# Kernel tuning notes

Hardware: AMD Instinct MI355X
Metric: run time of the kernel (lower is better)

The kernel has to match this reference:

```python
import jax, jax.numpy as jnp
import numpy as np

N = 30000       # nodes
E = 480000      # edges (before self-loops)
G = 64          # graphs in batch
IN = 128        # in_channels
HID = 128       # hidden_dim
HEADS = 4
NEG_SLOPE = 0.2


def gat_layer(x, src, dst, W, att_src, att_dst, b):
    """PyG-style GATConv: W [Fin, H*C], att_* [H, C], b [H*C]. Returns [N, H*C] (head concat)."""
    H, C = att_src.shape
    h = (x @ W).reshape(-1, H, C)                      # [N, H, C]
    a_s = jnp.einsum('nhc,hc->nh', h, att_src)         # [N, H]
    a_d = jnp.einsum('nhc,hc->nh', h, att_dst)
    e = jax.nn.leaky_relu(a_s[src] + a_d[dst], NEG_SLOPE)   # [Etot, H]
    # segment softmax over edges grouped by destination node
    m = jax.ops.segment_max(e, dst, num_segments=N)
    e = jnp.exp(e - m[dst])
    denom = jax.ops.segment_sum(e, dst, num_segments=N)
    alpha = e / (denom[dst] + 1e-16)                   # [Etot, H]
    msg = h[src] * alpha[:, :, None]                   # [Etot, H, C]
    out = jax.ops.segment_sum(msg, dst, num_segments=N)
    return out.reshape(-1, H * C) + b


def setup_inputs():
    key = jax.random.key(0)
    ks = jax.random.split(key, 13)
    s = 0.05
    x = jax.random.normal(ks[0], (N, IN), jnp.float32)
    edge_index = jax.random.randint(ks[1], (2, E), 0, N, dtype=jnp.int32)
    batch = jnp.sort(jax.random.randint(ks[2], (N,), 0, G, dtype=jnp.int32))
    return {
        'x': x,
        'edge_index': edge_index,
        'batch': batch,
        'W1': jax.random.normal(ks[3], (IN, HEADS * HID), jnp.float32) * s,
        'att_src1': jax.random.normal(ks[4], (HEADS, HID), jnp.float32) * s,
        'att_dst1': jax.random.normal(ks[5], (HEADS, HID), jnp.float32) * s,
        'b1': jnp.zeros((HEADS * HID,), jnp.float32),
        'W2': jax.random.normal(ks[6], (HEADS * HID, HID), jnp.float32) * s,
        'att_src2': jax.random.normal(ks[7], (1, HID), jnp.float32) * s,
        'att_dst2': jax.random.normal(ks[8], (1, HID), jnp.float32) * s,
        'b2': jnp.zeros((HID,), jnp.float32),
        'lin_w': jax.random.normal(ks[9], (HID, 1), jnp.float32) * s,
        'lin_b': jnp.zeros((1,), jnp.float32),
    }


def reference(x, edge_index, batch, W1, att_src1, att_dst1, b1, W2, att_src2, att_dst2, b2, lin_w, lin_b):
    # add self-loops (PyG GATConv default)
    loop = jnp.arange(N, dtype=edge_index.dtype)
    src = jnp.concatenate([edge_index[0], loop])
    dst = jnp.concatenate([edge_index[1], loop])

    h = gat_layer(x, src, dst, W1, att_src1, att_dst1, b1)   # [N, 4*HID]
    h = jax.nn.elu(h)
    h = gat_layer(h, src, dst, W2, att_src2, att_dst2, b2)   # [N, HID]
    h = jax.nn.elu(h)

    # global mean pool over graphs
    sums = jax.ops.segment_sum(h, batch, num_segments=G)     # [G, HID]
    cnts = jax.ops.segment_sum(jnp.ones((N,), h.dtype), batch, num_segments=G)
    pooled = sums / jnp.maximum(cnts, 1.0)[:, None]

    out = pooled @ lin_w + lin_b                             # [G, 1]
    return out.squeeze(-1)                                   # [G]
```

## Files before the change

### kernel.cpp

```cpp
#include <hip/hip_runtime.h>

#define NN    30000
#define EE    480000
#define ETOT  (EE + NN)
#define GG    64
#define IN_CH 128
#define HID   128
#define HEADS 4
#define F1    (HEADS * HID)
#define CAP   64

typedef __attribute__((ext_vector_type(8))) __bf16 bf16x8;
typedef __attribute__((ext_vector_type(4))) float  floatx4;
typedef __attribute__((ext_vector_type(2))) float  f32x2;

__device__ __forceinline__ float lrelu(float x) { return x > 0.f ? x : 0.2f * x; }
__device__ __forceinline__ float elu_f(float x) { return x > 0.f ? x : (expf(x) - 1.f); }
__device__ __forceinline__ unsigned short f2bf(float f) {
    unsigned int u = __float_as_uint(f);
    return (unsigned short)((u + 0x7FFFu + ((u >> 16) & 1u)) >> 16);
}
__device__ __forceinline__ float bf2f(unsigned short u) {
    return __uint_as_float(((unsigned int)u) << 16);
}
__device__ __forceinline__ f32x2 fma2(float a, f32x2 v, f32x2 acc) {
    f32x2 av = {a, a};
    return __builtin_elementwise_fma(av, v, acc);
}

__device__ __forceinline__ float wred_sum(float v) {
#pragma unroll
    for (int off = 32; off; off >>= 1) v += __shfl_xor(v, off);
    return v;
}

#define LDKC 136
__global__ __launch_bounds__(256) void gemm_bf16(const unsigned short* __restrict__ A, int lda, int zA,
                                                 const unsigned short* __restrict__ Bt, int zBt, int K,
                                                 unsigned short* __restrict__ C, int ldc, int zC,
                                                 const float* __restrict__ bias, int zBias,
                                                 int M, int do_elu)
{
    A  += (size_t)blockIdx.z * zA;
    Bt += (size_t)blockIdx.z * zBt;
    C  += (size_t)blockIdx.z * zC;
    const float* bias_p = bias ? bias + (size_t)blockIdx.z * zBias : nullptr;

    __shared__ unsigned short Bl[128 * LDKC];

    const int tid  = threadIdx.x;
    const int wave = tid >> 6, lane = tid & 63;
    const int quad = lane >> 4, l16 = lane & 15;
    const int bm = blockIdx.x * 128;

    floatx4 zf = {0.f, 0.f, 0.f, 0.f};
    floatx4 acc[2][8];
#pragma unroll
    for (int rt = 0; rt < 2; rt++)
#pragma unroll
        for (int ct = 0; ct < 8; ct++) acc[rt][ct] = zf;

    float bb[8];
#pragma unroll
    for (int ct = 0; ct < 8; ct++) bb[ct] = bias_p ? bias_p[ct * 16 + l16] : 0.f;

    const int r0 = bm + wave * 32 + l16;
    const int r1 = r0 + 16;

    for (int kc = 0; kc < K; kc += 128) {
        uint4 av[2][4];
#pragma unroll
        for (int kb = 0; kb < 4; kb++) {
            const int k = kc + kb * 32 + quad * 8;
            av[0][kb] = (r0 < M) ? *(const uint4*)(A + (size_t)r0 * lda + k) : uint4{0,0,0,0};
            av[1][kb] = (r1 < M) ? *(const uint4*)(A + (size_t)r1 * lda + k) : uint4{0,0,0,0};
        }

        if (kc) __syncthreads();
#pragma unroll
        for (int i = 0; i < 8; i++) {
            int j = i * 256 + tid;
            int n = j >> 4, ko = (j & 15) * 8;
            *(uint4*)&Bl[n * LDKC + ko] = *(const uint4*)(Bt + (size_t)n * K + kc + ko);
        }
        __syncthreads();

#pragma unroll
        for (int kb = 0; kb < 4; kb++) {
            bf16x8 bfr[8];
#pragma unroll
            for (int ct = 0; ct < 8; ct++)
                bfr[ct] = *(bf16x8*)&Bl[(ct * 16 + l16) * LDKC + kb * 32 + quad * 8];
            bf16x8 a0 = *(bf16x8*)&av[0][kb];
            bf16x8 a1 = *(bf16x8*)&av[1][kb];
#pragma unroll
            for (int ct = 0; ct < 8; ct++) {
                acc[0][ct] = __builtin_amdgcn_mfma_f32_16x16x32_bf16(a0, bfr[ct], acc[0][ct], 0, 0, 0);
                acc[1][ct] = __builtin_amdgcn_mfma_f32_16x16x32_bf16(a1, bfr[ct], acc[1][ct], 0, 0, 0);
            }
        }
    }

    __syncthreads();
    unsigned short* wls = Bl + wave * (16 * 128);
#pragma unroll
    for (int rt = 0; rt < 2; rt++) {
        if (rt) __builtin_amdgcn_wave_barrier();
#pragma unroll
        for (int ct = 0; ct < 8; ct++) {
#pragma unroll
            for (int reg = 0; reg < 4; reg++) {
                float v = acc[rt][ct][reg] + bb[ct];
                if (do_elu) v = elu_f(v);
                wls[(quad * 4 + reg) * 128 + ct * 16 + l16] = f2bf(v);
            }
        }
        __builtin_amdgcn_wave_barrier();
#pragma unroll
        for (int i = 0; i < 4; i++) {
            int j = i * 64 + lane;
            int rl = j >> 4, off = (j & 15) * 8;
            int row = bm + wave * 32 + rt * 16 + rl;
            if (row < M)
                *(uint4*)(C + (size_t)row * ldc + off) = *(uint4*)&wls[rl * 128 + off];
        }
    }
}

__global__ void cast_bf16_k(const float* __restrict__ src, unsigned short* __restrict__ dst, int npairs)
{
    int i = blockIdx.x * 256 + threadIdx.x;
    if (i < npairs) {
        float2 v = *(const float2*)(src + (size_t)i * 2);
        *(unsigned int*)(dst + (size_t)i * 2) =
            (unsigned)f2bf(v.x) | ((unsigned)f2bf(v.y) << 16);
    }
}

__global__ void prep_k(const float* __restrict__ W1, const float* __restrict__ W2,
                       const float* __restrict__ att_s, const float* __restrict__ att_d,
                       unsigned short* __restrict__ W1t, unsigned short* __restrict__ W2t,
                       float* __restrict__ wt)
{
    int b = blockIdx.x;
    if (b < 256) {
        int idx = b * 256 + threadIdx.x;
        int h = idx >> 14, rem = idx & 16383, n = rem >> 7, k = rem & 127;
        W1t[idx] = f2bf(W1[(size_t)k * F1 + h * 128 + n]);
    } else if (b < 512) {
        int idx = (b - 256) * 256 + threadIdx.x;
        int n = idx >> 9, k = idx & 511;
        W2t[idx] = f2bf(W2[(size_t)k * HID + n]);
    } else if (threadIdx.x < 128) {
        int q = b - 512;
        int h = q & 3, sd = q >> 2;
        int i = threadIdx.x;
        const float* att = (sd ? att_d : att_s) + h * 128;
        const float* wr = W1 + (size_t)i * F1 + h * 128;
        float acc = 0.f;
        for (int c = 0; c < 128; c++) acc = fmaf(wr[c], att[c], acc);
        wt[sd * 512 + h * 128 + i] = acc;
    }
}

__global__ __launch_bounds__(128) void score1_k(const float* __restrict__ x,
                                                const float* __restrict__ wt,
                                                float* __restrict__ a_s,
                                                float* __restrict__ a_d)
{
    __shared__ __align__(16) float swt[1024];
    int t = threadIdx.x;
    ((float4*)swt)[t]       = ((const float4*)wt)[t];
    ((float4*)swt)[t + 128] = ((const float4*)wt)[t + 128];
    __syncthreads();
    int node = blockIdx.x * 16 + (t >> 3);
    int q = t & 7;
    int h = q & 3, sd = q >> 2;
    if (node >= NN) return;
    const float4* xr = (const float4*)(x + (size_t)node * IN_CH);
    const float4* wr = (const float4*)(swt + sd * 512 + h * 128);
    float acc = 0.f;
#pragma unroll 4
    for (int c = 0; c < 32; c++) {
        float4 xv = xr[c], wv = wr[c];
        acc = fmaf(xv.x, wv.x, acc);
        acc = fmaf(xv.y, wv.y, acc);
        acc = fmaf(xv.z, wv.z, acc);
        acc = fmaf(xv.w, wv.w, acc);
    }
    if (sd == 0) a_s[node * 4 + h] = acc;
    else         a_d[node * 4 + h] = acc;
}

__global__ __launch_bounds__(256) void att_scores_k(const unsigned short* __restrict__ h16,
                                                    const float* __restrict__ w_s,
                                                    const float* __restrict__ w_d,
                                                    float* __restrict__ a_s,
                                                    float* __restrict__ a_d)
{
    int n = blockIdx.x * 4 + (threadIdx.x >> 6);
    if (n >= NN) return;
    int l = threadIdx.x & 63;
    const unsigned short* hr = h16 + (size_t)n * 128;
    float h0 = bf2f(hr[l]), h1 = bf2f(hr[l + 64]);
    float vs = wred_sum(h0 * w_s[l] + h1 * w_s[l + 64]);
    float vd = wred_sum(h0 * w_d[l] + h1 * w_d[l + 64]);
    if (l == 0) { a_s[n] = vs; a_d[n] = vd; }
}

__global__ void fill_k(const int* __restrict__ ei, int* __restrict__ deg, int* __restrict__ perm)
{
    int i = blockIdx.x * blockDim.x + threadIdx.x;
    if (i < ETOT) {
        int s, d;
        if (i < EE) { s = ei[i]; d = ei[EE + i]; }
        else        { s = i - EE; d = i - EE; }
        int p = atomicAdd(&deg[d], 1);
        if (p < CAP) perm[(size_t)d * CAP + p] = s;
    }
}

__global__ __launch_bounds__(256) void gat_agg1w(const unsigned short* __restrict__ x16,
                                                 const float* __restrict__ a_s,
                                                 const float* __restrict__ a_d,
                                                 const int* __restrict__ deg,
                                                 const int* __restrict__ perm,
                                                 unsigned short* __restrict__ agg)
{
    __shared__ int    sSrc[4][64];
    __shared__ __align__(16) float4 sE[4][64];
    const int wave = threadIdx.x >> 6;
    const int lane = threadIdx.x & 63;
    int n = blockIdx.x * 4 + wave;
    if (n >= NN) return;
    const int rem = min(deg[n], CAP);
    const float4 ad4 = *(const float4*)(a_d + (size_t)n * 4);

    f32x2 acc0 = {0.f, 0.f}, acc1 = {0.f, 0.f}, acc2 = {0.f, 0.f}, acc3 = {0.f, 0.f};
    float d0 = 0.f, d1 = 0.f, d2 = 0.f, d3 = 0.f;

    if (lane < rem) {
        int sj = perm[(size_t)n * CAP + lane];
        float4 av = *(const float4*)(a_s + (size_t)sj * 4);
        float e0 = __expf(lrelu(av.x + ad4.x));
        float e1 = __expf(lrelu(av.y + ad4.y));
        float e2 = __expf(lrelu(av.z + ad4.z));
        float e3 = __expf(lrelu(av.w + ad4.w));
        d0 = e0; d1 = e1; d2 = e2; d3 = e3;
        sSrc[wave][lane] = sj;
        sE[wave][lane] = make_float4(e0, e1, e2, e3);
    }
    __builtin_amdgcn_wave_barrier();
    for (int j = 0; j < rem; j++) {
        int s = sSrc[wave][j];
        float4 ev = sE[wave][j];
        unsigned int uv = *(const unsigned int*)(x16 + (size_t)s * IN_CH + lane * 2);
        f32x2 xv = { __uint_as_float(uv << 16), __uint_as_float(uv & 0xFFFF0000u) };
        acc0 = fma2(ev.x, xv, acc0);
        acc1 = fma2(ev.y, xv, acc1);
        acc2 = fma2(ev.z, xv, acc2);
        acc3 = fma2(ev.w, xv, acc3);
    }
    d0 = wred_sum(d0); d1 = wred_sum(d1); d2 = wred_sum(d2); d3 = wred_sum(d3);
    const float i0 = 1.f / (d0 + 1e-16f), i1 = 1.f / (d1 + 1e-16f);
    const float i2 = 1.f / (d2 + 1e-16f), i3 = 1.f / (d3 + 1e-16f);

    unsigned short* ag = agg + (size_t)n * F1 + lane * 2;
    *(unsigned int*)(ag + 0 * 128) = (unsigned)f2bf(acc0.x * i0) | ((unsigned)f2bf(acc0.y * i0) << 16);
    *(unsigned int*)(ag + 1 * 128) = (unsigned)f2bf(acc1.x * i1) | ((unsigned)f2bf(acc1.y * i1) << 16);
    *(unsigned int*)(ag + 2 * 128) = (unsigned)f2bf(acc2.x * i2) | ((unsigned)f2bf(acc2.y * i2) << 16);
    *(unsigned int*)(ag + 3 * 128) = (unsigned)f2bf(acc3.x * i3) | ((unsigned)f2bf(acc3.y * i3) << 16);
}

__global__ __launch_bounds__(256) void gat_agg2w(const unsigned short* __restrict__ h16,
                                                 const float* __restrict__ a_s,
                                                 const float* __restrict__ a_d,
                                                 const int* __restrict__ deg,
                                                 const int* __restrict__ perm,
                                                 const float* __restrict__ bias,
                                                 unsigned short* __restrict__ out16)
{
    int n = blockIdx.x * 4 + (threadIdx.x >> 6);
    if (n >= NN) return;
    const int lane = threadIdx.x & 63;
    const int rem = min(deg[n], CAP);
    const float ad = a_d[n];

    f32x2 acc = {0.f, 0.f};
    float den = 0.f;
    int sj = 0;
    float e = 0.f;
    if (lane < rem) {
        sj = perm[(size_t)n * CAP + lane];
        e = __expf(lrelu(a_s[sj] + ad));
        den = e;
    }
    for (int j = 0; j < rem; j++) {
        int   s = __shfl(sj, j);
        float a = __shfl(e, j);
        unsigned int uv = *(const unsigned int*)(h16 + (size_t)s * HID + lane * 2);
        f32x2 hv = { __uint_as_float(uv << 16), __uint_as_float(uv & 0xFFFF0000u) };
        acc = fma2(a, hv, acc);
    }
    den = wred_sum(den);
    const float inv = 1.f / (den + 1e-16f);
    float2 bb = *(const float2*)(bias + lane * 2);
    float v0 = elu_f(acc.x * inv + bb.x);
    float v1 = elu_f(acc.y * inv + bb.y);
    *(unsigned int*)(out16 + (size_t)n * HID + lane * 2) =
        (unsigned)f2bf(v0) | ((unsigned)f2bf(v1) << 16);
}

#define NPB 64
__global__ __launch_bounds__(128) void pool_seg_k(const unsigned short* __restrict__ out16,
                                                  const int* __restrict__ batch,
                                                  float* __restrict__ pooled,
                                                  float* __restrict__ cnt)
{
    int n0 = blockIdx.x * NPB;
    int n1 = min(n0 + NPB, NN);
    if (n0 >= n1) return;
    int t = threadIdx.x;
    int cur = batch[n0];
    float acc = 0.f;
    int count = 0;
    for (int n = n0; n < n1; n++) {
        int g = batch[n];
        if (g != cur) {
            atomicAdd(&pooled[cur * HID + t], acc);
            if (t == 0) atomicAdd(&cnt[cur], (float)count);
            acc = 0.f; count = 0; cur = g;
        }
        acc += bf2f(out16[(size_t)n * HID + t]);
        count++;
    }
    atomicAdd(&pooled[cur * HID + t], acc);
    if (t == 0) atomicAdd(&cnt[cur], (float)count);
}

__global__ void final_k(const float* __restrict__ pooled, const float* __restrict__ cnt,
                        const float* __restrict__ lw, const float* __restrict__ lb,
                        float* __restrict__ outp)
{
    int g = threadIdx.x;
    if (g < GG) {
        float acc = 0.f;
        for (int c = 0; c < HID; c++) acc += pooled[g * HID + c] * lw[c];
        float cc = fmaxf(cnt[g], 1.0f);
        outp[g] = acc / cc + lb[0];
    }
}

extern "C" void kernel_launch(void* const* d_in, const int* in_sizes, int n_in,
                              void* d_out, int out_size, void* d_ws, size_t ws_size,
                              hipStream_t stream)
{
    const float* x    = (const float*)d_in[0];
    const int*   ei   = (const int*)d_in[1];
    const int*   batch= (const int*)d_in[2];
    const float* W1   = (const float*)d_in[3];
    const float* as1w = (const float*)d_in[4];
    const float* ad1w = (const float*)d_in[5];
    const float* b1   = (const float*)d_in[6];
    const float* W2   = (const float*)d_in[7];
    const float* as2w = (const float*)d_in[8];
    const float* ad2w = (const float*)d_in[9];
    const float* b2   = (const float*)d_in[10];
    const float* lw   = (const float*)d_in[11];
    const float* lb   = (const float*)d_in[12];
    float* outp = (float*)d_out;

    char* w = (char*)d_ws;
    size_t off = 0;
    auto alloc = [&](size_t bytes) -> char* {
        char* p = w + off;
        off += (bytes + 255) & ~(size_t)255;
        return p;
    };
    char*  reg0   = alloc((size_t)NN * F1 * 4);
    char*  reg1   = alloc((size_t)NN * F1 * 2);
    unsigned short* x16 = (unsigned short*)alloc((size_t)NN * IN_CH * 2);
    unsigned short* W1t = (unsigned short*)alloc(65536 * 2);
    unsigned short* W2t = (unsigned short*)alloc(65536 * 2);
    float* wt1    = (float*)alloc(1024 * 4);
    float* a_s1   = (float*)alloc((size_t)NN * 4 * 4);
    float* a_d1   = (float*)alloc((size_t)NN * 4 * 4);
    float* a_s2   = (float*)alloc((size_t)NN * 4);
    float* a_d2   = (float*)alloc((size_t)NN * 4);
    int*   deg    = (int*)alloc((size_t)NN * 4);
    int*   perm   = (int*)alloc((size_t)NN * CAP * 4);
    float* pooled = (float*)alloc((size_t)GG * HID * 4);
    float* cnt    = (float*)alloc((size_t)GG * 4);

    unsigned short* agg16   = (unsigned short*)reg0;
    unsigned short* out116  = (unsigned short*)reg1;
    unsigned short* hh2_16  = (unsigned short*)reg0;
    unsigned short* out2_16 = (unsigned short*)reg0 + (size_t)NN * HID;

    hipMemsetAsync(deg, 0, (size_t)NN * 4, stream);
    hipMemsetAsync(pooled, 0, (size_t)GG * HID * 4 + 256, stream);

    cast_bf16_k<<<(NN * IN_CH / 2 + 255) / 256, 256, 0, stream>>>(x, x16, NN * IN_CH / 2);
    prep_k<<<520, 256, 0, stream>>>(W1, W2, as1w, ad1w, W1t, W2t, wt1);
    score1_k<<<(NN + 15) / 16, 128, 0, stream>>>(x, wt1, a_s1, a_d1);

    fill_k<<<(ETOT + 255) / 256, 256, 0, stream>>>(ei, deg, perm);

    gat_agg1w<<<(NN + 3) / 4, 256, 0, stream>>>(x16, a_s1, a_d1, deg, perm, agg16);
    const int MT = (NN + 127) / 128;
    gemm_bf16<<<dim3(MT, 1, 4), 256, 0, stream>>>(agg16, F1, 128, W1t, 128 * 128, 128,
                                                  out116, F1, 128, b1, 128, NN, 1);

    gemm_bf16<<<dim3(MT, 1, 1), 256, 0, stream>>>(out116, F1, 0, W2t, 0, F1,
                                                  hh2_16, HID, 0, nullptr, 0, NN, 0);
    att_scores_k<<<(NN + 3) / 4, 256, 0, stream>>>(hh2_16, as2w, ad2w, a_s2, a_d2);
    gat_agg2w<<<(NN + 3) / 4, 256, 0, stream>>>(hh2_16, a_s2, a_d2, deg, perm, b2, out2_16);

    pool_seg_k<<<(NN + NPB - 1) / NPB, 128, 0, stream>>>(out2_16, batch, pooled, cnt);
    final_k<<<1, 64, 0, stream>>>(pooled, cnt, lw, lb, outp);
}
```

Baseline: 263.7 us.

## Fuse memsets, bf16 cast, and layer-2 attention scores into neighboring kernels

Zeroing of deg and pooled/cnt moves into extra blocks of prep_k, the x→bf16 cast folds into score1_k, and the layer-2 attention-score dot products are computed in the second GEMM's epilogue from its LDS tile. The softmax denominators are now built from the broadcast per-edge values inside the aggregation loops, which removes the wave reductions. The aim is fewer kernel launches and fewer passes over global memory. In exchange, the GEMM epilogue does more work and the cast in score1_k uses scalar bf16 stores.

```diff
diff --git a/kernel.cpp b/kernel.cpp
--- a/kernel.cpp
+++ b/kernel.cpp
@@ -28,18 +28,16 @@
     return __builtin_elementwise_fma(av, v, acc);
 }
 
-__device__ __forceinline__ float wred_sum(float v) {
-#pragma unroll
-    for (int off = 32; off; off >>= 1) v += __shfl_xor(v, off);
-    return v;
-}
-
 #define LDKC 136
 __global__ __launch_bounds__(256) void gemm_bf16(const unsigned short* __restrict__ A, int lda, int zA,
                                                  const unsigned short* __restrict__ Bt, int zBt, int K,
                                                  unsigned short* __restrict__ C, int ldc, int zC,
                                                  const float* __restrict__ bias, int zBias,
-                                                 int M, int do_elu)
+                                                 int M, int do_elu,
+                                                 const float* __restrict__ ws,
+                                                 const float* __restrict__ wd,
+                                                 float* __restrict__ as_out,
+                                                 float* __restrict__ ad_out)
 {
     A  += (size_t)blockIdx.z * zA;
     Bt += (size_t)blockIdx.z * zBt;
@@ -124,23 +122,28 @@
             if (row < M)
                 *(uint4*)(C + (size_t)row * ldc + off) = *(uint4*)&wls[rl * 128 + off];
         }
-    }
-}
-
-__global__ void cast_bf16_k(const float* __restrict__ src, unsigned short* __restrict__ dst, int npairs)
-{
-    int i = blockIdx.x * 256 + threadIdx.x;
-    if (i < npairs) {
-        float2 v = *(const float2*)(src + (size_t)i * 2);
-        *(unsigned int*)(dst + (size_t)i * 2) =
-            (unsigned)f2bf(v.x) | ((unsigned)f2bf(v.y) << 16);
+        if (ws) {
+            int row = bm + wave * 32 + rt * 16 + l16;
+            const unsigned short* rowp = &wls[l16 * 128 + quad * 32];
+            float ps = 0.f, pd = 0.f;
+#pragma unroll
+            for (int jj = 0; jj < 32; jj++) {
+                float hv = bf2f(rowp[jj]);
+                ps = fmaf(hv, ws[quad * 32 + jj], ps);
+                pd = fmaf(hv, wd[quad * 32 + jj], pd);
+            }
+            ps += __shfl_xor(ps, 16); ps += __shfl_xor(ps, 32);
+            pd += __shfl_xor(pd, 16); pd += __shfl_xor(pd, 32);
+            if (quad == 0 && row < M) { as_out[row] = ps; ad_out[row] = pd; }
+        }
     }
 }
 
 __global__ void prep_k(const float* __restrict__ W1, const float* __restrict__ W2,
                        const float* __restrict__ att_s, const float* __restrict__ att_d,
                        unsigned short* __restrict__ W1t, unsigned short* __restrict__ W2t,
-                       float* __restrict__ wt)
+                       float* __restrict__ wt, int* __restrict__ deg,
+                       float* __restrict__ pooled_cnt)
 {
     int b = blockIdx.x;
     if (b < 256) {
@@ -151,61 +154,62 @@
         int idx = (b - 256) * 256 + threadIdx.x;
         int n = idx >> 9, k = idx & 511;
         W2t[idx] = f2bf(W2[(size_t)k * HID + n]);
-    } else if (threadIdx.x < 128) {
-        int q = b - 512;
-        int h = q & 3, sd = q >> 2;
-        int i = threadIdx.x;
-        const float* att = (sd ? att_d : att_s) + h * 128;
-        const float* wr = W1 + (size_t)i * F1 + h * 128;
-        float acc = 0.f;
-        for (int c = 0; c < 128; c++) acc = fmaf(wr[c], att[c], acc);
-        wt[sd * 512 + h * 128 + i] = acc;
+    } else if (b < 520) {
+        if (threadIdx.x < 128) {
+            int q = b - 512;
+            int h = q & 3, sd = q >> 2;
+            int i = threadIdx.x;
+            const float* att = (sd ? att_d : att_s) + h * 128;
+            const float* wr = W1 + (size_t)i * F1 + h * 128;
+            float acc = 0.f;
+            for (int c = 0; c < 128; c++) acc = fmaf(wr[c], att[c], acc);
+            wt[sd * 512 + h * 128 + i] = acc;
+        }
+    } else if (b < 638) {
+        int i = (b - 520) * 256 + threadIdx.x;
+        if (i < NN) deg[i] = 0;
+    } else {
+        int i = (b - 638) * 256 + threadIdx.x;
+        if (i < GG * HID + GG) pooled_cnt[i] = 0.f;
     }
 }
 
 __global__ __launch_bounds__(128) void score1_k(const float* __restrict__ x,
                                                 const float* __restrict__ wt,
                                                 float* __restrict__ a_s,
-                                                float* __restrict__ a_d)
+                                                float* __restrict__ a_d,
+                                                unsigned short* __restrict__ x16)
 {
     __shared__ __align__(16) float swt[1024];
     int t = threadIdx.x;
     ((float4*)swt)[t]       = ((const float4*)wt)[t];
     ((float4*)swt)[t + 128] = ((const float4*)wt)[t + 128];
     __syncthreads();
-    int node = blockIdx.x * 16 + (t >> 3);
+    const int node0 = blockIdx.x * 16;
+    int node = node0 + (t >> 3);
     int q = t & 7;
     int h = q & 3, sd = q >> 2;
-    if (node >= NN) return;
-    const float4* xr = (const float4*)(x + (size_t)node * IN_CH);
-    const float4* wr = (const float4*)(swt + sd * 512 + h * 128);
-    float acc = 0.f;
+    if (node < NN) {
+        const float4* xr = (const float4*)(x + (size_t)node * IN_CH);
+        const float4* wr = (const float4*)(swt + sd * 512 + h * 128);
+        float acc = 0.f;
 #pragma unroll 4
-    for (int c = 0; c < 32; c++) {
-        float4 xv = xr[c], wv = wr[c];
-        acc = fmaf(xv.x, wv.x, acc);
-        acc = fmaf(xv.y, wv.y, acc);
-        acc = fmaf(xv.z, wv.z, acc);
-        acc = fmaf(xv.w, wv.w, acc);
-    }
-    if (sd == 0) a_s[node * 4 + h] = acc;
-    else         a_d[node * 4 + h] = acc;
-}
-
-__global__ __launch_bounds__(256) void att_scores_k(const unsigned short* __restrict__ h16,
-                                                    const float* __restrict__ w_s,
-                                                    const float* __restrict__ w_d,
-                                                    float* __restrict__ a_s,
-                                                    float* __restrict__ a_d)
-{
-    int n = blockIdx.x * 4 + (threadIdx.x >> 6);
-    if (n >= NN) return;
-    int l = threadIdx.x & 63;
-    const unsigned short* hr = h16 + (size_t)n * 128;
-    float h0 = bf2f(hr[l]), h1 = bf2f(hr[l + 64]);
-    float vs = wred_sum(h0 * w_s[l] + h1 * w_s[l + 64]);
-    float vd = wred_sum(h0 * w_d[l] + h1 * w_d[l + 64]);
-    if (l == 0) { a_s[n] = vs; a_d[n] = vd; }
+        for (int c = 0; c < 32; c++) {
+            float4 xv = xr[c], wv = wr[c];
+            acc = fmaf(xv.x, wv.x, acc);
+            acc = fmaf(xv.y, wv.y, acc);
+            acc = fmaf(xv.z, wv.z, acc);
+            acc = fmaf(xv.w, wv.w, acc);
+        }
+        if (sd == 0) a_s[node * 4 + h] = acc;
+        else         a_d[node * 4 + h] = acc;
+    }
+#pragma unroll 4
+    for (int r = 0; r < 16; r++) {
+        int nr = node0 + r;
+        if (nr < NN)
+            x16[(size_t)nr * IN_CH + t] = f2bf(x[(size_t)nr * IN_CH + t]);
+    }
 }
 
 __global__ void fill_k(const int* __restrict__ ei, int* __restrict__ deg, int* __restrict__ perm)
@@ -237,23 +241,21 @@
     const float4 ad4 = *(const float4*)(a_d + (size_t)n * 4);
 
     f32x2 acc0 = {0.f, 0.f}, acc1 = {0.f, 0.f}, acc2 = {0.f, 0.f}, acc3 = {0.f, 0.f};
-    float d0 = 0.f, d1 = 0.f, d2 = 0.f, d3 = 0.f;
+    f32x2 den01 = {0.f, 0.f}, den23 = {0.f, 0.f};
 
     if (lane < rem) {
         int sj = perm[(size_t)n * CAP + lane];
         float4 av = *(const float4*)(a_s + (size_t)sj * 4);
-        float e0 = __expf(lrelu(av.x + ad4.x));
-        float e1 = __expf(lrelu(av.y + ad4.y));
-        float e2 = __expf(lrelu(av.z + ad4.z));
-        float e3 = __expf(lrelu(av.w + ad4.w));
-        d0 = e0; d1 = e1; d2 = e2; d3 = e3;
         sSrc[wave][lane] = sj;
-        sE[wave][lane] = make_float4(e0, e1, e2, e3);
+        sE[wave][lane] = make_float4(__expf(lrelu(av.x + ad4.x)), __expf(lrelu(av.y + ad4.y)),
+                                     __expf(lrelu(av.z + ad4.z)), __expf(lrelu(av.w + ad4.w)));
     }
     __builtin_amdgcn_wave_barrier();
     for (int j = 0; j < rem; j++) {
         int s = sSrc[wave][j];
         float4 ev = sE[wave][j];
+        den01 += (f32x2){ev.x, ev.y};
+        den23 += (f32x2){ev.z, ev.w};
         unsigned int uv = *(const unsigned int*)(x16 + (size_t)s * IN_CH + lane * 2);
         f32x2 xv = { __uint_as_float(uv << 16), __uint_as_float(uv & 0xFFFF0000u) };
         acc0 = fma2(ev.x, xv, acc0);
@@ -261,9 +263,8 @@
         acc2 = fma2(ev.z, xv, acc2);
         acc3 = fma2(ev.w, xv, acc3);
     }
-    d0 = wred_sum(d0); d1 = wred_sum(d1); d2 = wred_sum(d2); d3 = wred_sum(d3);
-    const float i0 = 1.f / (d0 + 1e-16f), i1 = 1.f / (d1 + 1e-16f);
-    const float i2 = 1.f / (d2 + 1e-16f), i3 = 1.f / (d3 + 1e-16f);
+    const float i0 = 1.f / (den01.x + 1e-16f), i1 = 1.f / (den01.y + 1e-16f);
+    const float i2 = 1.f / (den23.x + 1e-16f), i3 = 1.f / (den23.y + 1e-16f);
 
     unsigned short* ag = agg + (size_t)n * F1 + lane * 2;
     *(unsigned int*)(ag + 0 * 128) = (unsigned)f2bf(acc0.x * i0) | ((unsigned)f2bf(acc0.y * i0) << 16);
@@ -293,16 +294,15 @@
     if (lane < rem) {
         sj = perm[(size_t)n * CAP + lane];
         e = __expf(lrelu(a_s[sj] + ad));
-        den = e;
     }
     for (int j = 0; j < rem; j++) {
         int   s = __shfl(sj, j);
         float a = __shfl(e, j);
+        den += a;
         unsigned int uv = *(const unsigned int*)(h16 + (size_t)s * HID + lane * 2);
         f32x2 hv = { __uint_as_float(uv << 16), __uint_as_float(uv & 0xFFFF0000u) };
         acc = fma2(a, hv, acc);
     }
-    den = wred_sum(den);
     const float inv = 1.f / (den + 1e-16f);
     float2 bb = *(const float2*)(bias + lane * 2);
     float v0 = elu_f(acc.x * inv + bb.x);
@@ -389,31 +389,27 @@
     float* a_d2   = (float*)alloc((size_t)NN * 4);
     int*   deg    = (int*)alloc((size_t)NN * 4);
     int*   perm   = (int*)alloc((size_t)NN * CAP * 4);
-    float* pooled = (float*)alloc((size_t)GG * HID * 4);
-    float* cnt    = (float*)alloc((size_t)GG * 4);
+    float* pooled = (float*)alloc((size_t)(GG * HID + GG) * 4);
+    float* cnt    = pooled + GG * HID;
 
     unsigned short* agg16   = (unsigned short*)reg0;
     unsigned short* out116  = (unsigned short*)reg1;
     unsigned short* hh2_16  = (unsigned short*)reg0;
     unsigned short* out2_16 = (unsigned short*)reg0 + (size_t)NN * HID;
 
-    hipMemsetAsync(deg, 0, (size_t)NN * 4, stream);
-    hipMemsetAsync(pooled, 0, (size_t)GG * HID * 4 + 256, stream);
-
-    cast_bf16_k<<<(NN * IN_CH / 2 + 255) / 256, 256, 0, stream>>>(x, x16, NN * IN_CH / 2);
-    prep_k<<<520, 256, 0, stream>>>(W1, W2, as1w, ad1w, W1t, W2t, wt1);
-    score1_k<<<(NN + 15) / 16, 128, 0, stream>>>(x, wt1, a_s1, a_d1);
-
+    prep_k<<<671, 256, 0, stream>>>(W1, W2, as1w, ad1w, W1t, W2t, wt1, deg, pooled);
+    score1_k<<<(NN + 15) / 16, 128, 0, stream>>>(x, wt1, a_s1, a_d1, x16);
     fill_k<<<(ETOT + 255) / 256, 256, 0, stream>>>(ei, deg, perm);
 
     gat_agg1w<<<(NN + 3) / 4, 256, 0, stream>>>(x16, a_s1, a_d1, deg, perm, agg16);
     const int MT = (NN + 127) / 128;
     gemm_bf16<<<dim3(MT, 1, 4), 256, 0, stream>>>(agg16, F1, 128, W1t, 128 * 128, 128,
-                                                  out116, F1, 128, b1, 128, NN, 1);
+                                                  out116, F1, 128, b1, 128, NN, 1,
+                                                  nullptr, nullptr, nullptr, nullptr);
 
     gemm_bf16<<<dim3(MT, 1, 1), 256, 0, stream>>>(out116, F1, 0, W2t, 0, F1,
-                                                  hh2_16, HID, 0, nullptr, 0, NN, 0);
-    att_scores_k<<<(NN + 3) / 4, 256, 0, stream>>>(hh2_16, as2w, ad2w, a_s2, a_d2);
+                                                  hh2_16, HID, 0, nullptr, 0, NN, 0,
+                                                  as2w, ad2w, a_s2, a_d2);
     gat_agg2w<<<(NN + 3) / 4, 256, 0, stream>>>(hh2_16, a_s2, a_d2, deg, perm, b2, out2_16);
 
     pool_seg_k<<<(NN + NPB - 1) / NPB, 128, 0, stream>>>(out2_16, batch, pooled, cnt);
```

New measurement: 249.8 us. 5.3% less time.
